# Kernel optimization log

Measured on AMD Instinct MI355X. Metric: run time of the kernel, lower is better.

## Reference

```python
import jax, jax.numpy as jnp
import numpy as np

KH = KW = 9
STRIDE = 1
PAD = 4
DIL = 1


def _bilinear(img, py, px):
    """img: [C,H,W]; py, px: [kk,Ho,Wo] float sample coords -> [C,kk,Ho,Wo].
    Zero padding outside the image, matching DCNv2 semantics."""
    H, W = img.shape[-2], img.shape[-1]
    y0 = jnp.floor(py)
    x0 = jnp.floor(px)
    wy = py - y0  # fractional parts (carry the gradient wrt offsets)
    wx = px - x0

    def gather(yi, xi):
        valid = ((yi >= 0) & (yi < H) & (xi >= 0) & (xi < W)).astype(img.dtype)
        yc = jnp.clip(yi, 0, H - 1).astype(jnp.int32)
        xc = jnp.clip(xi, 0, W - 1).astype(jnp.int32)
        return img[:, yc, xc] * valid[None]

    v00 = gather(y0, x0)
    v01 = gather(y0, x0 + 1)
    v10 = gather(y0 + 1, x0)
    v11 = gather(y0 + 1, x0 + 1)
    return (v00 * (1 - wy) * (1 - wx) + v01 * (1 - wy) * wx
            + v10 * wy * (1 - wx) + v11 * wy * wx)


def setup_inputs() -> dict:
    key = jax.random.key(0)
    k1, k2, k3 = jax.random.split(key, 3)
    B, H, W = 2, 256, 256
    kk = KH * KW
    inp = jax.random.normal(k1, (B, 3, H, W), dtype=jnp.float32)
    offset = jax.random.normal(k2, (B, 2 * kk, H, W), dtype=jnp.float32)
    mask = jax.random.uniform(k3, (B, kk, H, W), dtype=jnp.float32)
    weight = jnp.ones((1, 1, KH, KW), dtype=jnp.float32) / kk  # frozen averaging kernel
    bias = jnp.zeros((1,), dtype=jnp.float32)
    return {"input": inp, "offset": offset, "mask": mask, "weight": weight, "bias": bias}


def reference(input, offset, mask, weight, bias):
    B, C, H, W = input.shape  # C = 3 * Ci (R,G,B chunks sharing weight/offset/mask)
    kk = KH * KW
    Ho = (H + 2 * PAD - DIL * (KH - 1) - 1) // STRIDE + 1
    Wo = (W + 2 * PAD - DIL * (KW - 1) - 1) // STRIDE + 1

    ky = jnp.repeat(jnp.arange(KH), KW)  # [kk]
    kx = jnp.tile(jnp.arange(KW), KH)
    base_y = (jnp.arange(Ho) * STRIDE - PAD)[None, :, None] + (ky * DIL)[:, None, None]  # [kk,Ho,1]
    base_x = (jnp.arange(Wo) * STRIDE - PAD)[None, None, :] + (kx * DIL)[:, None, None]  # [kk,1,Wo]

    off = offset.reshape(B, kk, 2, Ho, Wo)  # channel c = 2*k + {0: dy, 1: dx}
    py = base_y[None].astype(offset.dtype) + off[:, :, 0]  # [B,kk,Ho,Wo]
    px = base_x[None].astype(offset.dtype) + off[:, :, 1]

    # bilinear-sampled, modulated im2col: [B, C, kk, Ho, Wo]
    samples = jax.vmap(_bilinear)(input, py, px)
    val = samples * mask[:, None]

    Co, Ci = weight.shape[0], weight.shape[1]
    G = C // Ci  # 3 color groups, identical weight applied to each
    val = val.reshape(B, G, Ci, kk, Ho, Wo)
    wk = weight.reshape(Co, Ci, kk)
    out = jnp.einsum('bgckhw,ock->bgohw', val, wk) + bias[None, None, :, None, None]
    return out.reshape(B, G * Co, Ho, Wo)
```

## Files before the change

kernel.cpp:

```cpp
#include <hip/hip_runtime.h>
#include <hip/hip_fp16.h>

#define HH 256
#define WW 256
#define KK 81
#define PLANE (HH * WW)
#define SLACK 10
#define TR 21
#define TC 84
#define TAB (TR * TC)

__global__ __launch_bounds__(256) void pack_kernel(const float* __restrict__ in,
                                                   ushort4* __restrict__ img) {
    int idx = blockIdx.x * 256 + threadIdx.x;
    int b = idx >> 16;
    int pix = idx & 0xFFFF;
    const float* base = in + (size_t)b * 3 * PLANE + pix;
    _Float16 h0 = (_Float16)base[0];
    _Float16 h1 = (_Float16)base[PLANE];
    _Float16 h2 = (_Float16)base[2 * PLANE];
    ushort4 u;
    u.x = __builtin_bit_cast(unsigned short, h0);
    u.y = __builtin_bit_cast(unsigned short, h1);
    u.z = __builtin_bit_cast(unsigned short, h2);
    u.w = 0;
    img[idx] = u;
}

__device__ __forceinline__ void acc3(float w, unsigned int pa, unsigned int pb,
                                     float& ax, float& ay, float& az) {
    __half2 ha = __builtin_bit_cast(__half2, pa);
    __half2 hb = __builtin_bit_cast(__half2, pb);
    ax = fmaf(w, __low2float(ha), ax);
    ay = fmaf(w, __high2float(ha), ay);
    az = fmaf(w, __low2float(hb), az);
}

__global__ __launch_bounds__(256, 8) void dcn_kernel(
    const ushort4* __restrict__ img,
    const float* __restrict__ offset,
    const float* __restrict__ mask,
    const float* __restrict__ weight,
    const float* __restrict__ bias,
    float* __restrict__ out) {
    __shared__ uint2 tile[TAB];
    __shared__ float red[3][4][64];
    __shared__ float wk[KK];

    const int t = threadIdx.x;
    if (t < KK) wk[t] = weight[t];

    const int b = blockIdx.y;
    const int pix0 = blockIdx.x * 64;
    const int ho = pix0 >> 8;
    const int xb = (pix0 & 255) - SLACK;
    const int yb = ho - SLACK;
    const ushort4* ib = img + (size_t)b * PLANE;

    for (int i = 0; i < 7; ++i) {
        int cid = t + i * 256;
        if (cid < TAB) {
            int r = cid / TC;
            int c = cid - r * TC;
            int iy = yb + r;
            int ix = xb + c;
            unsigned int pa = 0, pb = 0;
            if (((unsigned)iy < (unsigned)HH) & ((unsigned)ix < (unsigned)WW)) {
                ushort4 u = ib[iy * WW + ix];
                pa = (unsigned int)u.x | ((unsigned int)u.y << 16);
                pb = (unsigned int)u.z;
            }
            tile[cid] = make_uint2(pa, pb);
        }
    }
    __syncthreads();

    const int w = t >> 6;
    const int lane = t & 63;
    const int wo = (pix0 & 255) + lane;
    const int pix = pix0 + lane;

    const int kbeg = w * 20 + (w ? 1 : 0);
    const int kend = kbeg + (w ? 20 : 21);
    int ky = kbeg / 9;
    int kx = kbeg - ky * 9;

    const float* op = offset + (size_t)b * 2 * KK * PLANE + (size_t)(2 * kbeg) * PLANE + pix;
    const float* mp = mask + (size_t)b * KK * PLANE + (size_t)kbeg * PLANE + pix;

    const float wof = (float)wo;
    float ax = 0.f, ay = 0.f, az = 0.f;

#pragma unroll 4
    for (int k = kbeg; k < kend; ++k) {
        float dy = op[0];
        float dx = op[PLANE];
        float m = mp[0] * wk[k];
        op += 2 * PLANE;
        mp += PLANE;

        float py = (float)(ho - 4 + ky) + dy;
        float px = wof + ((float)(kx - 4) + dx);
        float y0f = floorf(py), x0f = floorf(px);
        float wy = py - y0f, wx = px - x0f;
        int y0 = (int)y0f, x0 = (int)x0f;

        int r0 = y0 - yb;
        int c0 = x0 - xb;
        bool ok = ((unsigned)r0 < (TR - 1)) & ((unsigned)c0 < (TC - 1));

        float w1y = wy * m, w0y = m - w1y;
        float w00 = w0y * (1.f - wx), w01 = w0y * wx;
        float w10 = w1y * (1.f - wx), w11 = w1y * wx;

        uint2 q00, q01, q10, q11;
        if (__builtin_expect(__all(ok), 1)) {
            const uint2* p = &tile[r0 * TC + c0];
            q00 = p[0];
            q01 = p[1];
            q10 = p[TC];
            q11 = p[TC + 1];
        } else {
            if (ok) {
                const uint2* p = &tile[r0 * TC + c0];
                q00 = p[0];
                q01 = p[1];
                q10 = p[TC];
                q11 = p[TC + 1];
            } else {
                int y1 = y0 + 1, x1 = x0 + 1;
                float va0 = ((unsigned)y0 < (unsigned)HH) ? 1.f : 0.f;
                float va1 = ((unsigned)y1 < (unsigned)HH) ? 1.f : 0.f;
                float vb0 = ((unsigned)x0 < (unsigned)WW) ? 1.f : 0.f;
                float vb1 = ((unsigned)x1 < (unsigned)WW) ? 1.f : 0.f;
                w00 *= va0 * vb0;
                w01 *= va0 * vb1;
                w10 *= va1 * vb0;
                w11 *= va1 * vb1;
                int y0c = min(max(y0, 0), HH - 1);
                int y1c = min(max(y1, 0), HH - 1);
                int x0c = min(max(x0, 0), WW - 1);
                int x1c = min(max(x1, 0), WW - 1);
                ushort4 g00 = ib[y0c * WW + x0c];
                ushort4 g01 = ib[y0c * WW + x1c];
                ushort4 g10 = ib[y1c * WW + x0c];
                ushort4 g11 = ib[y1c * WW + x1c];
                q00 = make_uint2((unsigned int)g00.x | ((unsigned int)g00.y << 16), g00.z);
                q01 = make_uint2((unsigned int)g01.x | ((unsigned int)g01.y << 16), g01.z);
                q10 = make_uint2((unsigned int)g10.x | ((unsigned int)g10.y << 16), g10.z);
                q11 = make_uint2((unsigned int)g11.x | ((unsigned int)g11.y << 16), g11.z);
            }
        }

        acc3(w00, q00.x, q00.y, ax, ay, az);
        acc3(w01, q01.x, q01.y, ax, ay, az);
        acc3(w10, q10.x, q10.y, ax, ay, az);
        acc3(w11, q11.x, q11.y, ax, ay, az);

        if (++kx == 9) {
            kx = 0;
            ++ky;
        }
    }

    red[0][w][lane] = ax;
    red[1][w][lane] = ay;
    red[2][w][lane] = az;
    __syncthreads();

    if (t < 192) {
        const int c = t >> 6;
        const int l = t & 63;
        float s = red[c][0][l] + red[c][1][l] + red[c][2][l] + red[c][3][l] + bias[0];
        out[(size_t)b * 3 * PLANE + (size_t)c * PLANE + pix0 + l] = s;
    }
}

extern "C" void kernel_launch(void* const* d_in, const int* in_sizes, int n_in,
                              void* d_out, int out_size, void* d_ws, size_t ws_size,
                              hipStream_t stream) {
    const float* input = (const float*)d_in[0];
    const float* offset = (const float*)d_in[1];
    const float* mask = (const float*)d_in[2];
    const float* weight = (const float*)d_in[3];
    const float* bias = (const float*)d_in[4];
    float* out = (float*)d_out;

    const int B = in_sizes[0] / (3 * PLANE);
    ushort4* img = (ushort4*)d_ws;

    pack_kernel<<<B * PLANE / 256, 256, 0, stream>>>(input, img);
    dim3 grid(PLANE / 64, B);
    dcn_kernel<<<grid, 256, 0, stream>>>(img, offset, mask, weight, bias, out);
}
```

Before: 171.8 us.

## Prefetch all offsets and masks into registers before the tile barrier

Each wave now loads its 21 offset-y, offset-x and mask values into register arrays before the shared-tile barrier. These loads overlap with the tile fill and give many outstanding memory requests per thread. Work is split evenly at 21 taps per wave: waves other than the first start one tap early and zero that tap's mask so the shared tap is not counted twice. The sample loop is fully unrolled, and launch bounds drop to 4 blocks per CU to make room for the extra registers, which may reduce occupancy.

```diff
diff --git a/kernel.cpp b/kernel.cpp
--- a/kernel.cpp
+++ b/kernel.cpp
@@ -36,7 +36,7 @@
     az = fmaf(w, __low2float(hb), az);
 }
 
-__global__ __launch_bounds__(256, 8) void dcn_kernel(
+__global__ __launch_bounds__(256, 4) void dcn_kernel(
     const ushort4* __restrict__ img,
     const float* __restrict__ offset,
     const float* __restrict__ mask,
@@ -73,31 +73,36 @@
             tile[cid] = make_uint2(pa, pb);
         }
     }
-    __syncthreads();
 
     const int w = t >> 6;
     const int lane = t & 63;
-    const int wo = (pix0 & 255) + lane;
     const int pix = pix0 + lane;
-
-    const int kbeg = w * 20 + (w ? 1 : 0);
-    const int kend = kbeg + (w ? 20 : 21);
-    int ky = kbeg / 9;
-    int kx = kbeg - ky * 9;
+    const int kbeg = w * 20;
 
     const float* op = offset + (size_t)b * 2 * KK * PLANE + (size_t)(2 * kbeg) * PLANE + pix;
     const float* mp = mask + (size_t)b * KK * PLANE + (size_t)kbeg * PLANE + pix;
-
-    const float wof = (float)wo;
+    float pdy[21], pdx[21], pm[21];
+#pragma unroll
+    for (int j = 0; j < 21; ++j) {
+        pdy[j] = op[(size_t)(2 * j) * PLANE];
+        pdx[j] = op[(size_t)(2 * j + 1) * PLANE];
+        pm[j] = mp[(size_t)j * PLANE];
+    }
+
+    __syncthreads();
+
+    const float wof = (float)((pix0 & 255) + lane);
     float ax = 0.f, ay = 0.f, az = 0.f;
-
-#pragma unroll 4
-    for (int k = kbeg; k < kend; ++k) {
-        float dy = op[0];
-        float dx = op[PLANE];
-        float m = mp[0] * wk[k];
-        op += 2 * PLANE;
-        mp += PLANE;
+    int ky = 2 * w;
+    int kx = 2 * w;
+
+#pragma unroll
+    for (int j = 0; j < 21; ++j) {
+        const int k = kbeg + j;
+        float dy = pdy[j];
+        float dx = pdx[j];
+        float m = pm[j] * wk[k];
+        if (j == 0 && w != 0) m = 0.f;
 
         float py = (float)(ho - 4 + ky) + dy;
         float px = wof + ((float)(kx - 4) + dx);
```

Result: slower. 272.8 us (+58.8%).
